# Kernel tuning notes

Measured on AMD Instinct MI355X. Metric: run time of the kernel, lower is better.

## Reference

```python
import jax, jax.numpy as jnp
import numpy as np
from jax import lax

# ---- configuration (matches init_kwargs / input_specs) ----
N = 16384          # number of input points
F_IN = 64          # input feature dim
RATIO = 0.25       # fps ratio
M = int(N * RATIO) # number of sampled centers = 4096
RADIUS = 0.2       # radius for neighbor search
K = 64             # max_num_neighbors
F_HID = 64
F_OUT = 128


def _glorot(key, shape):
    fan_in = shape[0]
    return jax.random.normal(key, shape, jnp.float32) / jnp.sqrt(jnp.float32(fan_in))


def setup_inputs() -> dict:
    key = jax.random.key(0)
    ks = jax.random.split(key, 6)
    x = jax.random.normal(ks[0], (N, F_IN), jnp.float32)
    pos = jax.random.normal(ks[1], (N, 3), jnp.float32)
    batch = jnp.zeros((N,), jnp.int32)  # single point cloud
    # PointNet++ SA conv MLP: [F_IN+3 -> 64 -> 64 -> 128]
    W1 = _glorot(ks[2], (F_IN + 3, F_HID))
    b1 = jnp.zeros((F_HID,), jnp.float32)
    W2 = _glorot(ks[3], (F_HID, F_HID))
    b2 = jnp.zeros((F_HID,), jnp.float32)
    W3 = _glorot(ks[4], (F_HID, F_OUT))
    b3 = jnp.zeros((F_OUT,), jnp.float32)
    return {"x": x, "pos": pos, "batch": batch,
            "W1": W1, "b1": b1, "W2": W2, "b2": b2, "W3": W3, "b3": b3}


def fps(pos, m):
    """Farthest point sampling: returns m indices into pos [N,3]."""
    n = pos.shape[0]

    def step(carry, _):
        min_d2, last = carry
        d2 = jnp.sum((pos - pos[last]) ** 2, axis=-1)   # [N]
        min_d2 = jnp.minimum(min_d2, d2)
        nxt = jnp.argmax(min_d2).astype(jnp.int32)
        return (min_d2, nxt), last

    init = (jnp.full((n,), jnp.inf, pos.dtype), jnp.int32(0))
    _, idx = lax.scan(step, init, None, length=m)
    return idx  # [m]


def radius_neighbors(pos, pos_s, batch, batch_s, r, k):
    """For each center, k nearest neighbors within radius r (same batch).
    Returns nbr indices [M,K] and validity mask [M,K]."""
    d2 = jnp.sum((pos_s[:, None, :] - pos[None, :, :]) ** 2, axis=-1)  # [M,N]
    ok = (batch_s[:, None] == batch[None, :]) & (d2 <= r * r)
    score = jnp.where(ok, d2, jnp.inf)
    neg_vals, nbr = lax.top_k(-score, k)                # smallest distances first
    valid = jnp.isfinite(neg_vals)
    return nbr, valid


def reference(x, pos, batch, W1, b1, W2, b2, W3, b3):
    idx = fps(pos, M)                   # [M]
    pos_s = pos[idx]                    # [M,3]
    batch_s = batch[idx]                # [M]
    nbr, valid = radius_neighbors(pos, pos_s, batch, batch_s, RADIUS, K)
    # gather neighbor features and relative positions
    rel = pos[nbr] - pos_s[:, None, :]                      # [M,K,3]
    h = jnp.concatenate([x[nbr], rel], axis=-1)             # [M,K,F_IN+3]
    # per-edge MLP (PointNetConv message)
    h = jax.nn.relu(h @ W1 + b1)
    h = jax.nn.relu(h @ W2 + b2)
    h = jax.nn.relu(h @ W3 + b3)                            # [M,K,F_OUT]
    # max aggregation over valid neighbors (center is always its own neighbor)
    h = jnp.where(valid[..., None], h, -jnp.inf)
    out = jnp.max(h, axis=1)                                # [M,F_OUT]
    return out, pos_s, batch_s
```

## Files before the change

### kernel.cpp

```cpp
#include <hip/hip_runtime.h>

#define N_PTS 16384
#define M_CTR 4096
#define K_NBR 64
#define F_OUT 128
#define CAP   256
#define FS    68
#define NCELL 4096
#define NBKT  512

__device__ __forceinline__ float d2_exact(float ax, float ay, float az,
                                          float bx, float by, float bz) {
  float dx = __fsub_rn(ax, bx);
  float dy = __fsub_rn(ay, by);
  float dz = __fsub_rn(az, bz);
  return __fadd_rn(__fadd_rn(__fmul_rn(dx, dx), __fmul_rn(dy, dy)),
                   __fmul_rn(dz, dz));
}

__device__ __forceinline__ unsigned long long wave_max_u64(unsigned long long v) {
  int lo = (int)(unsigned)v;
  int hi = (int)(unsigned)(v >> 32);
#define DPPSTEP64(ctrl, rm)                                                    \
  {                                                                            \
    int tlo = __builtin_amdgcn_update_dpp(lo, lo, ctrl, rm, 0xf, false);       \
    int thi = __builtin_amdgcn_update_dpp(hi, hi, ctrl, rm, 0xf, false);       \
    unsigned long long cur =                                                   \
        ((unsigned long long)(unsigned)hi << 32) | (unsigned)lo;               \
    unsigned long long oth =                                                   \
        ((unsigned long long)(unsigned)thi << 32) | (unsigned)tlo;             \
    if (oth > cur) { lo = tlo; hi = thi; }                                     \
  }
  DPPSTEP64(0x111, 0xf) DPPSTEP64(0x112, 0xf) DPPSTEP64(0x114, 0xf)
  DPPSTEP64(0x118, 0xf) DPPSTEP64(0x142, 0xa) DPPSTEP64(0x143, 0xc)
#undef DPPSTEP64
  const unsigned rlo = (unsigned)__builtin_amdgcn_readlane(lo, 63);
  const unsigned rhi = (unsigned)__builtin_amdgcn_readlane(hi, 63);
  return ((unsigned long long)rhi << 32) | rlo;
}

__global__ void __launch_bounds__(1024) prep_bbox_kernel(const float* __restrict__ pos,
                                                         float* __restrict__ bbox,
                                                         int* __restrict__ hist) {
  const int tid = threadIdx.x;
  __shared__ float sred[6][16];
  float mn[3] = {INFINITY, INFINITY, INFINITY};
  float mx[3] = {-INFINITY, -INFINITY, -INFINITY};
  for (int p = tid; p < N_PTS; p += 1024) {
#pragma unroll
    for (int d = 0; d < 3; ++d) {
      float v = pos[3 * p + d];
      mn[d] = fminf(mn[d], v);
      mx[d] = fmaxf(mx[d], v);
    }
  }
#pragma unroll
  for (int off = 32; off > 0; off >>= 1) {
#pragma unroll
    for (int d = 0; d < 3; ++d) {
      mn[d] = fminf(mn[d], __shfl_xor(mn[d], off));
      mx[d] = fmaxf(mx[d], __shfl_xor(mx[d], off));
    }
  }
  if ((tid & 63) == 0) {
    const int w = tid >> 6;
#pragma unroll
    for (int d = 0; d < 3; ++d) { sred[d][w] = mn[d]; sred[3 + d][w] = mx[d]; }
  }
  __syncthreads();
  if (tid == 0) {
#pragma unroll
    for (int d = 0; d < 3; ++d) {
      float a = sred[d][0], b = sred[3 + d][0];
      for (int w = 1; w < 16; ++w) { a = fminf(a, sred[d][w]); b = fmaxf(b, sred[3 + d][w]); }
      bbox[d] = a; bbox[3 + d] = b;
    }
  }
  for (int i = tid; i < NCELL; i += 1024) hist[i] = 0;
}

__device__ __forceinline__ int spread4(int v) {
  return (v & 1) | ((v & 2) << 2) | ((v & 4) << 4) | ((v & 8) << 6);
}

__global__ void __launch_bounds__(256) prep_cell_kernel(const float* __restrict__ pos,
                                                        const float* __restrict__ bbox,
                                                        int* __restrict__ cellid,
                                                        int* __restrict__ hist) {
  const int p = blockIdx.x * 256 + threadIdx.x;
  const float x = pos[3 * p], y = pos[3 * p + 1], z = pos[3 * p + 2];
  const float x0 = bbox[0], y0 = bbox[1], z0 = bbox[2];
  const float sx = 16.0f / fmaxf(bbox[3] - x0, 1e-20f);
  const float sy = 16.0f / fmaxf(bbox[4] - y0, 1e-20f);
  const float sz = 16.0f / fmaxf(bbox[5] - z0, 1e-20f);
  int cx = min(15, (int)((x - x0) * sx));
  int cy = min(15, (int)((y - y0) * sy));
  int cz = min(15, (int)((z - z0) * sz));
  const int c = spread4(cx) | (spread4(cy) << 1) | (spread4(cz) << 2);
  cellid[p] = c;
  atomicAdd(&hist[c], 1);
}

__global__ void __launch_bounds__(1024) prep_scan_kernel(const int* __restrict__ hist,
                                                         int* __restrict__ cursor) {
  __shared__ int tsum[1024];
  const int t = threadIdx.x;
  const int v0 = hist[4 * t + 0], v1 = hist[4 * t + 1];
  const int v2 = hist[4 * t + 2], v3 = hist[4 * t + 3];
  const int s = v0 + v1 + v2 + v3;
  int acc = s;
  tsum[t] = acc;
  __syncthreads();
  for (int off = 1; off < 1024; off <<= 1) {
    int add = (t >= off) ? tsum[t - off] : 0;
    __syncthreads();
    acc += add;
    tsum[t] = acc;
    __syncthreads();
  }
  int base = acc - s;
  cursor[4 * t + 0] = base;
  cursor[4 * t + 1] = base + v0;
  cursor[4 * t + 2] = base + v0 + v1;
  cursor[4 * t + 3] = base + v0 + v1 + v2;
}

__global__ void __launch_bounds__(256) prep_scatter_kernel(const float* __restrict__ pos,
                                                           const int* __restrict__ cellid,
                                                           int* __restrict__ cursor,
                                                           float4* __restrict__ gxyz) {
  const int p = blockIdx.x * 256 + threadIdx.x;
  const int c = cellid[p];
  const int dst = atomicAdd(&cursor[c], 1);
  gxyz[dst] = make_float4(pos[3 * p + 0], pos[3 * p + 1], pos[3 * p + 2],
                          __int_as_float(p));
}

__global__ void __launch_bounds__(64) prep_bktbox_kernel(const float4* __restrict__ gxyz,
                                                         float* __restrict__ gbox) {
  const int lane = threadIdx.x;
  const float4 q = gxyz[blockIdx.x * 64 + lane];
  float mnx = q.x, mxx = q.x, mny = q.y, mxy = q.y, mnz = q.z, mxz = q.z;
#pragma unroll
  for (int off = 16; off > 0; off >>= 1) {
    mnx = fminf(mnx, __shfl_xor(mnx, off)); mxx = fmaxf(mxx, __shfl_xor(mxx, off));
    mny = fminf(mny, __shfl_xor(mny, off)); mxy = fmaxf(mxy, __shfl_xor(mxy, off));
    mnz = fminf(mnz, __shfl_xor(mnz, off)); mxz = fmaxf(mxz, __shfl_xor(mxz, off));
  }
  if ((lane & 31) == 0) {
    const int b = blockIdx.x * 2 + (lane >> 5);
    gbox[b * 8 + 0] = mnx; gbox[b * 8 + 1] = mxx;
    gbox[b * 8 + 2] = mny; gbox[b * 8 + 3] = mxy;
    gbox[b * 8 + 4] = mnz; gbox[b * 8 + 5] = mxz;
    gbox[b * 8 + 6] = 0.0f; gbox[b * 8 + 7] = 0.0f;
  }
}

__global__ void __launch_bounds__(512) fps_bucket_kernel(
    const float* __restrict__ pos, const float4* __restrict__ gxyz,
    const float* __restrict__ gbox,
    int* __restrict__ idx_out, float* __restrict__ pos_s_out,
    float* __restrict__ batch_s_out) {
  __shared__ float s_md[N_PTS];
  __shared__ unsigned long long s_pk[NBKT];
  __shared__ int s_wl[NBKT];
  __shared__ unsigned long long s_rec[8];
  __shared__ int s_cnt;
  __shared__ int s_sidx[M_CTR];
  const int tid = threadIdx.x;
  const int lane = tid & 63, wave = tid >> 6;

  for (int i = tid; i < N_PTS; i += 512) s_md[i] = INFINITY;
  const float bx0 = gbox[tid * 8 + 0], bx1 = gbox[tid * 8 + 1];
  const float by0 = gbox[tid * 8 + 2], by1 = gbox[tid * 8 + 3];
  const float bz0 = gbox[tid * 8 + 4], bz1 = gbox[tid * 8 + 5];
  unsigned long long mpk = ((unsigned long long)0x7f800000u << 32);
  s_pk[tid] = mpk;
  if (tid == 0) s_cnt = 0;
  float cx = pos[0], cy = pos[1], cz = pos[2];
  int cIdx = 0;
  __syncthreads();

  for (int t = 0; t < M_CTR; ++t) {
    if (tid == 0) s_sidx[t] = cIdx;

    const float rMax = __uint_as_float((unsigned)(mpk >> 32));
    float dxl = fmaxf(fmaxf(bx0 - cx, cx - bx1), 0.0f);
    float dyl = fmaxf(fmaxf(by0 - cy, cy - by1), 0.0f);
    float dzl = fmaxf(fmaxf(bz0 - cz, cz - bz1), 0.0f);
    const bool flag = (dxl * dxl + dyl * dyl + dzl * dzl) * 0.99999f < rMax;
    const unsigned long long ball = __ballot(flag);
    int base = 0;
    if (lane == 0) base = atomicAdd(&s_cnt, __popcll(ball));
    base = __shfl(base, 0);
    if (flag) {
      const int pre = __popcll(ball & ((1ull << lane) - 1ull));
      s_wl[base + pre] = tid;
    }
    __syncthreads();

    const int nf = s_cnt;
    const int total = nf << 5;
    for (int bi = 0; bi < total; bi += 512) {
      const int idx = bi + tid;
      if (idx < total) {
        const int b = s_wl[idx >> 5];
        const int p = (b << 5) | (idx & 31);
        const float4 q = gxyz[p];
        const float old = s_md[p];
        const float nmd = fminf(old, d2_exact(q.x, q.y, q.z, cx, cy, cz));
        s_md[p] = nmd;
        unsigned long long lpk =
            ((unsigned long long)__float_as_uint(nmd) << 32) |
            ((unsigned long long)(16383u - (unsigned)__float_as_int(q.w)) << 14) |
            (unsigned)p;
#pragma unroll
        for (int mH = 1; mH < 32; mH <<= 1) {
          const unsigned olo =
              (unsigned)__shfl_xor((int)(unsigned)lpk, mH, 32);
          const unsigned ohi =
              (unsigned)__shfl_xor((int)(unsigned)(lpk >> 32), mH, 32);
          const unsigned long long o = ((unsigned long long)ohi << 32) | olo;
          if (o > lpk) lpk = o;
        }
        if ((idx & 31) == 0) s_pk[b] = lpk;
      }
    }
    __syncthreads();
    if (tid == 0) s_cnt = 0;

    mpk = s_pk[tid];
    const unsigned long long wpk = wave_max_u64(mpk);
    if (lane == 0) s_rec[wave] = wpk;
    __syncthreads();
    unsigned long long bpk = s_rec[0];
#pragma unroll
    for (int w = 1; w < 8; ++w) {
      const unsigned long long r = s_rec[w];
      if (r > bpk) bpk = r;
    }
    cIdx = 16383 - (int)((bpk >> 14) & 16383u);
    const int posn = (int)(bpk & 16383u);
    const float4 cq = gxyz[posn];
    cx = cq.x; cy = cq.y; cz = cq.z;
  }
  __syncthreads();
  for (int i = tid; i < M_CTR; i += 512) {
    const int si = s_sidx[i];
    idx_out[i] = si;
    pos_s_out[3 * i + 0] = pos[3 * si + 0];
    pos_s_out[3 * i + 1] = pos[3 * si + 1];
    pos_s_out[3 * i + 2] = pos[3 * si + 2];
    batch_s_out[i] = 0.0f;
  }
}

__global__ void __launch_bounds__(256) nbr_kernel(const float* __restrict__ pos,
                                                  const int* __restrict__ idx,
                                                  int* __restrict__ nbr) {
  const int m = blockIdx.x, tid = threadIdx.x;
  __shared__ int s_cnt;
  __shared__ float s_d2[CAP];
  __shared__ int s_idx[CAP];
  if (tid == 0) s_cnt = 0;
  const int cen = idx[m];
  const float cx = pos[3 * cen + 0], cy = pos[3 * cen + 1], cz = pos[3 * cen + 2];
  __syncthreads();
  const float RR = 0.04f;
  for (int i = 0; i < N_PTS / 256; ++i) {
    const int p = tid + 256 * i;
    float d2 = d2_exact(pos[3 * p], pos[3 * p + 1], pos[3 * p + 2], cx, cy, cz);
    if (d2 <= RR) {
      int slot = atomicAdd(&s_cnt, 1);
      if (slot < CAP) { s_d2[slot] = d2; s_idx[slot] = p; }
    }
  }
  __syncthreads();
  const int cnt = s_cnt;
  if (cnt <= K_NBR) {
    if (tid < K_NBR) nbr[m * K_NBR + tid] = (tid < cnt) ? s_idx[tid] : cen;
  } else {
    const int n = cnt < CAP ? cnt : CAP;
    if (tid >= n) { s_d2[tid] = INFINITY; s_idx[tid] = 0x7fffffff; }
    __syncthreads();
    for (int k = 2; k <= CAP; k <<= 1) {
      for (int j = k >> 1; j > 0; j >>= 1) {
        const int ixj = tid ^ j;
        if (ixj > tid) {
          float da = s_d2[tid], db = s_d2[ixj];
          int ia = s_idx[tid], ib = s_idx[ixj];
          bool gt = (da > db) || (da == db && ia > ib);
          bool asc = ((tid & k) == 0);
          if (gt == asc) {
            s_d2[tid] = db; s_d2[ixj] = da;
            s_idx[tid] = ib; s_idx[ixj] = ia;
          }
        }
        __syncthreads();
      }
    }
    if (tid < K_NBR) nbr[m * K_NBR + tid] = s_idx[tid];
  }
}

__device__ __forceinline__ void mlp_layer(const float (*__restrict__ A)[FS],
                                          const float (*__restrict__ W)[64],
                                          int K, int e0, int c0, float acc[4][4]) {
#pragma unroll
  for (int j = 0; j < 4; ++j)
#pragma unroll
    for (int i = 0; i < 4; ++i) acc[j][i] = W[67][c0 + i];
#pragma unroll 4
  for (int k = 0; k < K; ++k) {
    const float4 w = *(const float4*)&W[k][c0];
    const float a0 = A[e0 + 0][k], a1 = A[e0 + 1][k];
    const float a2 = A[e0 + 2][k], a3 = A[e0 + 3][k];
    acc[0][0] = fmaf(a0, w.x, acc[0][0]); acc[0][1] = fmaf(a0, w.y, acc[0][1]);
    acc[0][2] = fmaf(a0, w.z, acc[0][2]); acc[0][3] = fmaf(a0, w.w, acc[0][3]);
    acc[1][0] = fmaf(a1, w.x, acc[1][0]); acc[1][1] = fmaf(a1, w.y, acc[1][1]);
    acc[1][2] = fmaf(a1, w.z, acc[1][2]); acc[1][3] = fmaf(a1, w.w, acc[1][3]);
    acc[2][0] = fmaf(a2, w.x, acc[2][0]); acc[2][1] = fmaf(a2, w.y, acc[2][1]);
    acc[2][2] = fmaf(a2, w.z, acc[2][2]); acc[2][3] = fmaf(a2, w.w, acc[2][3]);
    acc[3][0] = fmaf(a3, w.x, acc[3][0]); acc[3][1] = fmaf(a3, w.y, acc[3][1]);
    acc[3][2] = fmaf(a3, w.z, acc[3][2]); acc[3][3] = fmaf(a3, w.w, acc[3][3]);
  }
#pragma unroll
  for (int j = 0; j < 4; ++j)
#pragma unroll
    for (int i = 0; i < 4; ++i) acc[j][i] = fmaxf(acc[j][i], 0.0f);
}

__global__ void __launch_bounds__(512) mlp_kernel(
    const float* __restrict__ x, const float* __restrict__ pos,
    const int* __restrict__ nbr, const float* __restrict__ pos_s,
    const float* __restrict__ W1, const float* __restrict__ b1,
    const float* __restrict__ W2, const float* __restrict__ b2,
    const float* __restrict__ W3, const float* __restrict__ b3,
    float* __restrict__ out) {
  __shared__ float Fb[2][64][FS];
  __shared__ float Wb[FS][64];
  __shared__ float Pb[2][16][64];
  __shared__ int s_nbr[128];
  const int t = threadIdx.x;
  const int m0 = blockIdx.x * 2;

  if (t < 128) s_nbr[t] = nbr[m0 * K_NBR + t];
  __syncthreads();

  {
    const int ge = t >> 2, wch = ge >> 6, e = ge & 63, c16 = (t & 3) * 16;
    const int n = s_nbr[ge];
    const float4* src = (const float4*)(x + n * 64 + c16);
    float4* dst = (float4*)(&Fb[wch][e][c16]);
    dst[0] = src[0]; dst[1] = src[1]; dst[2] = src[2]; dst[3] = src[3];
  }
  if (t < 128) {
    const int wch = t >> 6, e = t & 63;
    const int n = s_nbr[t];
    const float cx = pos_s[(m0 + wch) * 3 + 0];
    const float cy = pos_s[(m0 + wch) * 3 + 1];
    const float cz = pos_s[(m0 + wch) * 3 + 2];
    Fb[wch][e][64] = pos[3 * n + 0] - cx;
    Fb[wch][e][65] = pos[3 * n + 1] - cy;
    Fb[wch][e][66] = pos[3 * n + 2] - cz;
    Fb[wch][e][67] = 0.0f;
  }
  for (int i = t; i < 67 * 64; i += 512) ((float*)Wb)[i] = W1[i];
  if (t < 64) Wb[67][t] = b1[t];
  __syncthreads();

  const int wch = t >> 8, tt = t & 255;
  const int e0 = (tt >> 4) << 2, c0 = (tt & 15) << 2;
  float acc[4][4];

  mlp_layer(Fb[wch], Wb, 67, e0, c0, acc);
  __syncthreads();
#pragma unroll
  for (int j = 0; j < 4; ++j)
#pragma unroll
    for (int i = 0; i < 4; ++i) Fb[wch][e0 + j][c0 + i] = acc[j][i];
  for (int i = t; i < 64 * 64; i += 512) ((float*)Wb)[i] = W2[i];
  if (t < 64) Wb[67][t] = b2[t];
  __syncthreads();

  mlp_layer(Fb[wch], Wb, 64, e0, c0, acc);
  __syncthreads();
#pragma unroll
  for (int j = 0; j < 4; ++j)
#pragma unroll
    for (int i = 0; i < 4; ++i) Fb[wch][e0 + j][c0 + i] = acc[j][i];

  for (int h = 0; h < 2; ++h) {
    for (int i = t; i < 64 * 64; i += 512)
      ((float*)Wb)[i] = W3[(i >> 6) * 128 + h * 64 + (i & 63)];
    if (t < 64) Wb[67][t] = b3[h * 64 + t];
    __syncthreads();
    mlp_layer(Fb[wch], Wb, 64, e0, c0, acc);
#pragma unroll
    for (int i = 0; i < 4; ++i) {
      float v = fmaxf(fmaxf(acc[0][i], acc[1][i]), fmaxf(acc[2][i], acc[3][i]));
      Pb[wch][tt >> 4][c0 + i] = v;
    }
    __syncthreads();
    if (tt < 64) {
      float v = Pb[wch][0][tt];
#pragma unroll
      for (int r = 1; r < 16; ++r) v = fmaxf(v, Pb[wch][r][tt]);
      out[(m0 + wch) * F_OUT + h * 64 + tt] = v;
    }
    __syncthreads();
  }
}

extern "C" void kernel_launch(void* const* d_in, const int* in_sizes, int n_in,
                              void* d_out, int out_size, void* d_ws, size_t ws_size,
                              hipStream_t stream) {
  const float* x   = (const float*)d_in[0];
  const float* pos = (const float*)d_in[1];
  const float* W1 = (const float*)d_in[3];
  const float* b1 = (const float*)d_in[4];
  const float* W2 = (const float*)d_in[5];
  const float* b2 = (const float*)d_in[6];
  const float* W3 = (const float*)d_in[7];
  const float* b3 = (const float*)d_in[8];

  float* out     = (float*)d_out;
  float* pos_s   = out + M_CTR * F_OUT;
  float* batch_s = pos_s + M_CTR * 3;

  int*    idx    = (int*)d_ws;
  int*    nbr    = idx + M_CTR;
  float*  bbox   = (float*)(nbr + M_CTR * K_NBR);
  int*    hist   = (int*)(bbox + 8);
  int*    cursor = hist + NCELL;
  int*    cellid = cursor + NCELL;
  float4* gxyz   = (float4*)(cellid + N_PTS);
  float*  gbox   = (float*)hist;

  prep_bbox_kernel<<<1, 1024, 0, stream>>>(pos, bbox, hist);
  prep_cell_kernel<<<N_PTS / 256, 256, 0, stream>>>(pos, bbox, cellid, hist);
  prep_scan_kernel<<<1, 1024, 0, stream>>>(hist, cursor);
  prep_scatter_kernel<<<N_PTS / 256, 256, 0, stream>>>(pos, cellid, cursor, gxyz);
  prep_bktbox_kernel<<<NBKT / 2, 64, 0, stream>>>(gxyz, gbox);
  fps_bucket_kernel<<<1, 512, 0, stream>>>(pos, gxyz, gbox, idx, pos_s, batch_s);
  nbr_kernel<<<M_CTR, 256, 0, stream>>>(pos, idx, nbr);
  mlp_kernel<<<M_CTR / 2, 512, 0, stream>>>(x, pos, nbr, pos_s,
                                            W1, b1, W2, b2, W3, b3, out);
}
```

Before: 6.051 ms.

## Remove second barrier per FPS step via redundant per-wave global max

Every wave now reads all 512 bucket maxima from shared memory and reduces them itself. This replaces the per-wave partial results followed by a second __syncthreads, so each iteration needs one barrier fewer. The bucket counter is double-buffered so it can be reset without an extra barrier, and the winning point's xyz is cached in shared memory instead of being reloaded from global memory. The intra-bucket reduction uses DPP for the first two butterfly steps, and the final redundant iteration is skipped. The cost is eight shared loads per thread per step and a risk from writer races when two lanes tie on the packed key, although the keys are unique.

```diff
diff --git a/kernel.cpp b/kernel.cpp
--- a/kernel.cpp
+++ b/kernel.cpp
@@ -37,6 +37,31 @@
   const unsigned rlo = (unsigned)__builtin_amdgcn_readlane(lo, 63);
   const unsigned rhi = (unsigned)__builtin_amdgcn_readlane(hi, 63);
   return ((unsigned long long)rhi << 32) | rlo;
+}
+
+__device__ __forceinline__ unsigned long long bucket_bfly_max_u64(
+    unsigned long long red) {
+  {
+    int lo = (int)(unsigned)red, hi = (int)(unsigned)(red >> 32);
+    int tlo = __builtin_amdgcn_update_dpp(lo, lo, 0xB1, 0xf, 0xf, false);
+    int thi = __builtin_amdgcn_update_dpp(hi, hi, 0xB1, 0xf, 0xf, false);
+    unsigned long long o =
+        ((unsigned long long)(unsigned)thi << 32) | (unsigned)tlo;
+    if (o > red) red = o;
+    lo = (int)(unsigned)red; hi = (int)(unsigned)(red >> 32);
+    tlo = __builtin_amdgcn_update_dpp(lo, lo, 0x4E, 0xf, 0xf, false);
+    thi = __builtin_amdgcn_update_dpp(hi, hi, 0x4E, 0xf, 0xf, false);
+    o = ((unsigned long long)(unsigned)thi << 32) | (unsigned)tlo;
+    if (o > red) red = o;
+  }
+#pragma unroll
+  for (int mH = 4; mH < 32; mH <<= 1) {
+    const unsigned olo = (unsigned)__shfl_xor((int)(unsigned)red, mH);
+    const unsigned ohi = (unsigned)__shfl_xor((int)(unsigned)(red >> 32), mH);
+    const unsigned long long o = ((unsigned long long)ohi << 32) | olo;
+    if (o > red) red = o;
+  }
+  return red;
 }
 
 __global__ void __launch_bounds__(1024) prep_bbox_kernel(const float* __restrict__ pos,
@@ -163,9 +188,9 @@
     float* __restrict__ batch_s_out) {
   __shared__ float s_md[N_PTS];
   __shared__ unsigned long long s_pk[NBKT];
+  __shared__ float4 s_wxyz[NBKT];
   __shared__ int s_wl[NBKT];
-  __shared__ unsigned long long s_rec[8];
-  __shared__ int s_cnt;
+  __shared__ int s_cnt[2];
   __shared__ int s_sidx[M_CTR];
   const int tid = threadIdx.x;
   const int lane = tid & 63, wave = tid >> 6;
@@ -176,13 +201,15 @@
   const float bz0 = gbox[tid * 8 + 4], bz1 = gbox[tid * 8 + 5];
   unsigned long long mpk = ((unsigned long long)0x7f800000u << 32);
   s_pk[tid] = mpk;
-  if (tid == 0) s_cnt = 0;
+  if (tid < 2) s_cnt[tid] = 0;
   float cx = pos[0], cy = pos[1], cz = pos[2];
   int cIdx = 0;
   __syncthreads();
 
   for (int t = 0; t < M_CTR; ++t) {
     if (tid == 0) s_sidx[t] = cIdx;
+    if (t == M_CTR - 1) break;
+    const int par = t & 1;
 
     const float rMax = __uint_as_float((unsigned)(mpk >> 32));
     float dxl = fmaxf(fmaxf(bx0 - cx, cx - bx1), 0.0f);
@@ -191,15 +218,16 @@
     const bool flag = (dxl * dxl + dyl * dyl + dzl * dzl) * 0.99999f < rMax;
     const unsigned long long ball = __ballot(flag);
     int base = 0;
-    if (lane == 0) base = atomicAdd(&s_cnt, __popcll(ball));
-    base = __shfl(base, 0);
+    if (lane == 0) base = atomicAdd(&s_cnt[par], __popcll(ball));
+    base = __builtin_amdgcn_readfirstlane(base);
     if (flag) {
       const int pre = __popcll(ball & ((1ull << lane) - 1ull));
       s_wl[base + pre] = tid;
     }
     __syncthreads();
-
-    const int nf = s_cnt;
+    if (tid == 0) s_cnt[par ^ 1] = 0;
+
+    const int nf = s_cnt[par];
     const int total = nf << 5;
     for (int bi = 0; bi < total; bi += 512) {
       const int idx = bi + tid;
@@ -207,41 +235,32 @@
         const int b = s_wl[idx >> 5];
         const int p = (b << 5) | (idx & 31);
         const float4 q = gxyz[p];
-        const float old = s_md[p];
-        const float nmd = fminf(old, d2_exact(q.x, q.y, q.z, cx, cy, cz));
+        const float nmd = fminf(s_md[p], d2_exact(q.x, q.y, q.z, cx, cy, cz));
         s_md[p] = nmd;
-        unsigned long long lpk =
+        const unsigned long long own =
             ((unsigned long long)__float_as_uint(nmd) << 32) |
             ((unsigned long long)(16383u - (unsigned)__float_as_int(q.w)) << 14) |
             (unsigned)p;
-#pragma unroll
-        for (int mH = 1; mH < 32; mH <<= 1) {
-          const unsigned olo =
-              (unsigned)__shfl_xor((int)(unsigned)lpk, mH, 32);
-          const unsigned ohi =
-              (unsigned)__shfl_xor((int)(unsigned)(lpk >> 32), mH, 32);
-          const unsigned long long o = ((unsigned long long)ohi << 32) | olo;
-          if (o > lpk) lpk = o;
+        const unsigned long long red = bucket_bfly_max_u64(own);
+        if (own == red) {
+          s_pk[b] = red;
+          s_wxyz[b] = make_float4(q.x, q.y, q.z, 0.0f);
         }
-        if ((idx & 31) == 0) s_pk[b] = lpk;
       }
     }
     __syncthreads();
-    if (tid == 0) s_cnt = 0;
-
-    mpk = s_pk[tid];
-    const unsigned long long wpk = wave_max_u64(mpk);
-    if (lane == 0) s_rec[wave] = wpk;
-    __syncthreads();
-    unsigned long long bpk = s_rec[0];
-#pragma unroll
-    for (int w = 1; w < 8; ++w) {
-      const unsigned long long r = s_rec[w];
-      if (r > bpk) bpk = r;
-    }
+
+    unsigned long long loc = 0ULL;
+#pragma unroll
+    for (int k = 0; k < 8; ++k) {
+      const unsigned long long v = s_pk[(k << 6) | lane];
+      if (k == wave) mpk = v;
+      if (v > loc) loc = v;
+    }
+    const unsigned long long bpk = wave_max_u64(loc);
     cIdx = 16383 - (int)((bpk >> 14) & 16383u);
     const int posn = (int)(bpk & 16383u);
-    const float4 cq = gxyz[posn];
+    const float4 cq = s_wxyz[posn >> 5];
     cx = cq.x; cy = cq.y; cz = cq.z;
   }
   __syncthreads();
```

Result: no change. 6.070 ms (+0.3%).
